# Kernel optimization log

Measured on AMD Instinct MI355X. Metric: run time of the kernel, lower is better.

## Reference

```python
import jax, jax.numpy as jnp
import numpy as np

EPS = 1e-10
B, S, D, K = 8, 2048, 512, 1024
TEMP = 1.0  # quantizer temperature set to 1.0 in SQVAE.__init__


def _ln(x, g, b):
    m = x.mean(-1, keepdims=True)
    v = x.var(-1, keepdims=True)
    return (x - m) / jnp.sqrt(v + 1e-5) * g + b


def _mlp(x, w1, b1, g1, be1, w2, b2, g2, be2):
    # feed_forward: Linear -> ReLU -> LayerNorm, twice (MLPLayers=2)
    h = _ln(jax.nn.relu(x @ w1 + b1), g1, be1)
    return _ln(jax.nn.relu(h @ w2 + b2), g2, be2)


def setup_inputs() -> dict:
    key = jax.random.key(0)
    ks = jax.random.split(key, 20)
    W = 0.04  # small init scale to keep distances / softmax well-conditioned
    p = lambda k, sh, s=1.0: jax.random.normal(k, sh, dtype=jnp.float32) * s
    return {
        'x': p(ks[0], (B, S, D)),
        'gumbel_u': jax.random.uniform(ks[1], (B * S, K), dtype=jnp.float32),
        'enc_w1': p(ks[2], (D, D), W), 'enc_b1': jnp.zeros(D, jnp.float32),
        'enc_g1': jnp.ones(D, jnp.float32), 'enc_be1': jnp.zeros(D, jnp.float32),
        'enc_w2': p(ks[3], (D, D), W), 'enc_b2': jnp.zeros(D, jnp.float32),
        'enc_g2': jnp.ones(D, jnp.float32), 'enc_be2': jnp.zeros(D, jnp.float32),
        'dec_w1': p(ks[4], (D, D), W), 'dec_b1': jnp.zeros(D, jnp.float32),
        'dec_g1': jnp.ones(D, jnp.float32), 'dec_be1': jnp.zeros(D, jnp.float32),
        'dec_w2': p(ks[5], (D, D), W), 'dec_b2': jnp.zeros(D, jnp.float32),
        'dec_g2': jnp.ones(D, jnp.float32), 'dec_be2': jnp.zeros(D, jnp.float32),
        'codebook': p(ks[6], (K, D)),
        'log_param_q': jnp.zeros((), jnp.float32),
    }


def reference(x, gumbel_u, enc_w1, enc_b1, enc_g1, enc_be1, enc_w2, enc_b2, enc_g2, enc_be2,
              dec_w1, dec_b1, dec_g1, dec_be1, dec_w2, dec_b2, dec_g2, dec_be2,
              codebook, log_param_q):
    bs, seq, d = x.shape
    z = _mlp(x, enc_w1, enc_b1, enc_g1, enc_be1, enc_w2, enc_b2, enc_g2, enc_be2)
    # gaussian_1: log_var_q = 0 -> var_q = exp(log_param_q_scalar)
    var_q = jnp.exp(log_param_q)
    w = 0.5 / jnp.clip(var_q, 1e-10)  # 0.5 * precision_q (scalar)
    zf = z.reshape(-1, d)  # [N, D]
    # cdist^2 style distance, scaled by weight -> logits [N, K]
    dist = w * (jnp.sum(zf * zf, axis=1, keepdims=True)
                + jnp.sum(codebook * codebook, axis=1)
                - 2.0 * zf @ codebook.T)
    logit = -dist
    logp = jax.nn.log_softmax(logit, axis=-1)
    probs = jnp.exp(logp)
    # gumbel-softmax sample (train path), noise provided as uniform input
    g = -jnp.log(-jnp.log(gumbel_u + EPS) + EPS)
    encodings = jax.nn.softmax((logit + g) / TEMP, axis=-1)
    z_q = (encodings @ codebook).reshape(bs, seq, d)
    kld_discrete = jnp.sum(probs * logp) / bs
    kld_continuous = jnp.mean(jnp.sum((z - z_q) ** 2 * w, axis=(1, 2)))
    loss = kld_discrete + kld_continuous
    avg_probs = jnp.mean(jax.lax.stop_gradient(probs), axis=0)
    perplexity = jnp.exp(-jnp.sum(avg_probs * jnp.log(avg_probs + 1e-7)))
    x_rec = _mlp(z_q, dec_w1, dec_b1, dec_g1, dec_be1, dec_w2, dec_b2, dec_g2, dec_be2)
    return x_rec, loss, perplexity
```

## Files before the change

### kernel.cpp

```cpp
#include <hip/hip_runtime.h>
#include <math.h>

#define NROWS 16384
#define DIM   512
#define KCODE 1024

typedef __attribute__((ext_vector_type(8))) __bf16 bf16x8;
typedef __attribute__((ext_vector_type(4))) float f32x4;

__device__ __forceinline__ float wave_reduce_sum(float v) {
  #pragma unroll
  for (int m = 1; m < 64; m <<= 1) v += __shfl_xor(v, m, 64);
  return v;
}
__device__ __forceinline__ float wave_reduce_max(float v) {
  #pragma unroll
  for (int m = 1; m < 64; m <<= 1) v = fmaxf(v, __shfl_xor(v, m, 64));
  return v;
}
__device__ __forceinline__ unsigned short f2bf(float f) {
  union { float f; unsigned u; } v; v.f = f;
  unsigned r = v.u + 0x7FFFu + ((v.u >> 16) & 1u);
  return (unsigned short)(r >> 16);
}
__device__ __forceinline__ float bf2f(unsigned short h) {
  union { unsigned u; float f; } v; v.u = ((unsigned)h) << 16;
  return v.f;
}
__device__ __forceinline__ uint4 pack8(const float* x) {
  uint4 r;
  r.x = (unsigned)f2bf(x[0]) | ((unsigned)f2bf(x[1]) << 16);
  r.y = (unsigned)f2bf(x[2]) | ((unsigned)f2bf(x[3]) << 16);
  r.z = (unsigned)f2bf(x[4]) | ((unsigned)f2bf(x[5]) << 16);
  r.w = (unsigned)f2bf(x[6]) | ((unsigned)f2bf(x[7]) << 16);
  return r;
}

__device__ __forceinline__ void glds16(const void* g, void* lds) {
  __builtin_amdgcn_global_load_lds(
      (const __attribute__((address_space(1))) unsigned int*)g,
      (__attribute__((address_space(3))) unsigned int*)lds, 16, 0, 0);
}

__global__ __launch_bounds__(512, 2) void dist_fused(
    const unsigned short* __restrict__ zhp, const unsigned short* __restrict__ zlp,
    const unsigned short* __restrict__ cbh, const unsigned short* __restrict__ cbl,
    const float* __restrict__ znorm, const float* __restrict__ cnorm,
    const float* __restrict__ lpq, float* __restrict__ outf) {
  __shared__ char smem[65536];
  const int t = threadIdx.x;
  const int l = t & 63, w = t >> 6;
  const int wm = w >> 2, wn = w & 3;
  const int b = blockIdx.x;
  const int xcd = b & 7, j = b >> 3;
  const int m0 = (xcd * 8 + j / 4) * 256;
  const int n0 = (j % 4) * 256;

  f32x4 acc[8][4];
  #pragma unroll
  for (int i = 0; i < 8; ++i)
    #pragma unroll
    for (int jj = 0; jj < 4; ++jj) acc[i][jj] = (f32x4){0.f, 0.f, 0.f, 0.f};

  const int row = l & 15;
  const int kcol = (l >> 4) * 8;
  const size_t aLo = (size_t)(m0 + w * 16 + row) * 512 + kcol;
  const size_t aHi = aLo + (size_t)128 * 512;

  const unsigned short* __restrict__ cbhB = cbh + (size_t)(n0 + row) * 512 + kcol;
  const unsigned short* __restrict__ cblB = cbl + (size_t)(n0 + row) * 512 + kcol;

  auto issue = [&](int s) {
    char* hb = smem + (s & 1) * 32768;
    const int kt = s * 32;
    glds16(zhp + aLo + kt, hb + w * 1024);
    glds16(zhp + aHi + kt, hb + (w + 8) * 1024);
    glds16(zlp + aLo + kt, hb + 16384 + w * 1024);
    glds16(zlp + aHi + kt, hb + 16384 + (w + 8) * 1024);
  };

  issue(0);
  #pragma unroll 1
  for (int s = 0; s < 16; ++s) {
    const int kt2 = s * 32;
    bf16x8 bh[4], blf[4];
    #pragma unroll
    for (int i = 0; i < 4; ++i) {
      bh[i]  = *(const bf16x8*)(cbhB + (size_t)(wn * 4 + i) * 8192 + kt2);
      blf[i] = *(const bf16x8*)(cblB + (size_t)(wn * 4 + i) * 8192 + kt2);
    }
    if (s + 1 < 16) {
      issue(s + 1);
      asm volatile("s_waitcnt vmcnt(12)" ::: "memory");
    } else {
      asm volatile("s_waitcnt vmcnt(8)" ::: "memory");
    }
    __builtin_amdgcn_s_barrier();
    const char* hb = smem + (s & 1) * 32768;
    bf16x8 af[8];
    #pragma unroll
    for (int i = 0; i < 8; ++i)
      af[i] = *(const bf16x8*)(hb + (wm * 8 + i) * 1024 + l * 16);
    #pragma unroll
    for (int mi = 0; mi < 8; ++mi)
      #pragma unroll
      for (int ni = 0; ni < 4; ++ni) {
        acc[mi][ni] = __builtin_amdgcn_mfma_f32_16x16x32_bf16(af[mi], bh[ni], acc[mi][ni], 0, 0, 0);
        acc[mi][ni] = __builtin_amdgcn_mfma_f32_16x16x32_bf16(af[mi], blf[ni], acc[mi][ni], 0, 0, 0);
      }
    #pragma unroll
    for (int i = 0; i < 8; ++i)
      af[i] = *(const bf16x8*)(hb + 16384 + (wm * 8 + i) * 1024 + l * 16);
    #pragma unroll
    for (int mi = 0; mi < 8; ++mi)
      #pragma unroll
      for (int ni = 0; ni < 4; ++ni)
        acc[mi][ni] = __builtin_amdgcn_mfma_f32_16x16x32_bf16(af[mi], bh[ni], acc[mi][ni], 0, 0, 0);
    __builtin_amdgcn_s_barrier();
  }

  float* slab = (float*)(smem + w * 4352);
  const int q = l >> 4, c16 = l & 15;
  const int c4 = (l & 15) * 4;
  const float wq = 0.5f / fmaxf(expf(lpq[0]), 1e-10f);

  #pragma unroll
  for (int mi = 0; mi < 8; ++mi) {
    __syncthreads();
    #pragma unroll
    for (int ni = 0; ni < 4; ++ni)
      #pragma unroll
      for (int r = 0; r < 4; ++r)
        slab[(q * 4 + r) * 68 + ni * 16 + c16] = acc[mi][ni][r];
    __syncthreads();
    #pragma unroll
    for (int pp = 0; pp < 4; ++pp) {
      const int rw = pp * 4 + q;
      const float4 v4 = *(const float4*)&slab[rw * 68 + c4];
      const int m = m0 + wm * 128 + mi * 16 + rw;
      const int nc = n0 + wn * 64 + c4;
      const float zn = znorm[m];
      const float4 cn = *(const float4*)&cnorm[nc];
      float4 o;
      o.x = -wq * (zn + cn.x - 2.f * v4.x);
      o.y = -wq * (zn + cn.y - 2.f * v4.y);
      o.z = -wq * (zn + cn.z - 2.f * v4.z);
      o.w = -wq * (zn + cn.w - 2.f * v4.w);
      *(float4*)&outf[(size_t)m * KCODE + nc] = o;
    }
  }
}

template <int EPI, int K, int N, int LDA, int MROWS>
__global__ __launch_bounds__(512, 2) void gemm256(
    const unsigned short* A0, const unsigned short* B0,
    const float* __restrict__ znorm, const float* __restrict__ cnorm,
    const float* __restrict__ lpq,
    const unsigned short* __restrict__ zh, const unsigned short* __restrict__ zl,
    float* __restrict__ kldc,
    unsigned short* __restrict__ outb, float* __restrict__ outf) {
  __shared__ char smem[34816];
  const int t = threadIdx.x;
  const int l = t & 63, w = t >> 6;
  const int wm = w >> 2, wn = w & 3;
  const int NTN = N / 256;
  const int b = blockIdx.x;
  const int xcd = b & 7, j = b >> 3;
  const int MT_PER_XCD = (MROWS / 256) / 8;
  const int m0 = (xcd * MT_PER_XCD + j / NTN) * 256;
  const int n0 = (j % NTN) * 256;

  f32x4 acc[8][4];
  #pragma unroll
  for (int i = 0; i < 8; ++i)
    #pragma unroll
    for (int jj = 0; jj < 4; ++jj) acc[i][jj] = (f32x4){0.f, 0.f, 0.f, 0.f};

  const int row = l & 15;
  const int kcol = (l >> 4) * 8;
  const size_t oA0 = (size_t)(m0 + w * 16 + row) * LDA + kcol;
  const size_t oA1 = oA0 + (size_t)128 * LDA;
  const unsigned short* __restrict__ Bb = B0 + (size_t)(n0 + row) * K + kcol;

  constexpr int NSTEP = K / 32;

  auto issue = [&](int ss) {
    char* hb = smem + (ss & 1) * 16384;
    const int kt = ss * 32;
    glds16(A0 + oA0 + kt, hb + w * 1024);
    glds16(A0 + oA1 + kt, hb + (w + 8) * 1024);
  };

  issue(0);
  #pragma unroll 1
  for (int s = 0; s < NSTEP; ++s) {
    const int kt2 = s * 32;
    bf16x8 bfr[4];
    #pragma unroll
    for (int i = 0; i < 4; ++i)
      bfr[i] = *(const bf16x8*)(Bb + (size_t)(wn * 4 + i) * 16 * K + kt2);
    if (s + 1 < NSTEP) {
      issue(s + 1);
      asm volatile("s_waitcnt vmcnt(6)" ::: "memory");
    } else {
      asm volatile("s_waitcnt vmcnt(4)" ::: "memory");
    }
    __builtin_amdgcn_s_barrier();
    const char* hb = smem + (s & 1) * 16384;
    bf16x8 af[8];
    #pragma unroll
    for (int i = 0; i < 8; ++i)
      af[i] = *(const bf16x8*)(hb + (wm * 8 + i) * 1024 + l * 16);
    #pragma unroll
    for (int mi = 0; mi < 8; ++mi)
      #pragma unroll
      for (int ni = 0; ni < 4; ++ni)
        acc[mi][ni] = __builtin_amdgcn_mfma_f32_16x16x32_bf16(af[mi], bfr[ni], acc[mi][ni], 0, 0, 0);
    __builtin_amdgcn_s_barrier();
  }

  float* slab = (float*)(smem + w * 4352);
  const int q = l >> 4, c16 = l & 15;
  const int c4 = (l & 15) * 4;
  const float wq = 0.5f / fmaxf(expf(lpq[0]), 1e-10f);
  float local = 0.f;

  #pragma unroll
  for (int mi = 0; mi < 8; ++mi) {
    __syncthreads();
    #pragma unroll
    for (int ni = 0; ni < 4; ++ni)
      #pragma unroll
      for (int r = 0; r < 4; ++r)
        slab[(q * 4 + r) * 68 + ni * 16 + c16] = acc[mi][ni][r];
    __syncthreads();
    #pragma unroll
    for (int pp = 0; pp < 4; ++pp) {
      const int rw = pp * 4 + q;
      const float4 v4 = *(const float4*)&slab[rw * 68 + c4];
      float v[4] = {v4.x, v4.y, v4.z, v4.w};
      const int m = m0 + wm * 128 + mi * 16 + rw;
      const int nc = n0 + wn * 64 + c4;
      if (EPI == 1) {
        const float zn = znorm[m];
        const float4 cn = *(const float4*)&cnorm[nc];
        float4 o;
        o.x = -wq * (zn + cn.x - 2.f * v[0]);
        o.y = -wq * (zn + cn.y - 2.f * v[1]);
        o.z = -wq * (zn + cn.z - 2.f * v[2]);
        o.w = -wq * (zn + cn.w - 2.f * v[3]);
        *(float4*)&outf[(size_t)m * N + nc] = o;
      } else {
        const uint2 h2 = *(const uint2*)&zh[(size_t)m * N + nc];
        const uint2 l2 = *(const uint2*)&zl[(size_t)m * N + nc];
        const float z0 = bf2f((unsigned short)(h2.x & 0xFFFF)) + bf2f((unsigned short)(l2.x & 0xFFFF));
        const float z1 = bf2f((unsigned short)(h2.x >> 16))    + bf2f((unsigned short)(l2.x >> 16));
        const float z2 = bf2f((unsigned short)(h2.y & 0xFFFF)) + bf2f((unsigned short)(l2.y & 0xFFFF));
        const float z3 = bf2f((unsigned short)(h2.y >> 16))    + bf2f((unsigned short)(l2.y >> 16));
        const float d0 = z0 - v[0], d1 = z1 - v[1], d2 = z2 - v[2], d3 = z3 - v[3];
        local += d0 * d0 + d1 * d1 + d2 * d2 + d3 * d3;
        uint2 st;
        st.x = (unsigned)f2bf(v[0]) | ((unsigned)f2bf(v[1]) << 16);
        st.y = (unsigned)f2bf(v[2]) | ((unsigned)f2bf(v[3]) << 16);
        *(uint2*)&outb[(size_t)m * N + nc] = st;
      }
    }
  }
  if (EPI == 2) {
    local = wave_reduce_sum(local) * wq;
    if (l == 0) atomicAdd(kldc, local);
  }
}

template <int EPI, int K, int N, int LDA>
__global__ __launch_bounds__(256) void gemm_bt(
    const unsigned short* A0, const unsigned short* B0,
    const float* __restrict__ bias,
    unsigned short* __restrict__ outb) {
  __shared__ char smem[17408];
  const int t = threadIdx.x;
  const int l = t & 63, w = t >> 6;
  const int wm = w >> 1, wn = w & 1;
  const int NTN = N / 128;
  const int b = blockIdx.x;
  const int xcd = b & 7;
  const int j = b >> 3;
  const int m0 = (xcd * 16 + j / NTN) * 128;
  const int n0 = (j % NTN) * 128;

  f32x4 acc[4][4];
  #pragma unroll
  for (int i = 0; i < 4; ++i)
    #pragma unroll
    for (int jj = 0; jj < 4; ++jj) acc[i][jj] = (f32x4){0.f, 0.f, 0.f, 0.f};

  const int row = l & 15;
  const int kcol = (l >> 4) * 8;
  const size_t oA0 = (size_t)(m0 + w * 16 + row) * LDA + kcol;
  const size_t oA1 = oA0 + (size_t)64 * LDA;
  const unsigned short* __restrict__ Bb = B0 + (size_t)(n0 + row) * K + kcol;

  constexpr int NSTEP = K / 32;

  auto issue = [&](int ss) {
    char* hb = smem + (ss & 1) * 8192;
    const int kt = ss * 32;
    glds16(A0 + oA0 + kt, hb + w * 1024);
    glds16(A0 + oA1 + kt, hb + (w + 4) * 1024);
  };

  issue(0);
  #pragma unroll 1
  for (int s = 0; s < NSTEP; ++s) {
    const int kt2 = s * 32;
    bf16x8 bfr[4];
    #pragma unroll
    for (int i = 0; i < 4; ++i)
      bfr[i] = *(const bf16x8*)(Bb + (size_t)(wn * 4 + i) * 16 * K + kt2);
    if (s + 1 < NSTEP) {
      issue(s + 1);
      asm volatile("s_waitcnt vmcnt(6)" ::: "memory");
    } else {
      asm volatile("s_waitcnt vmcnt(4)" ::: "memory");
    }
    __builtin_amdgcn_s_barrier();
    const char* hb = smem + (s & 1) * 8192;
    bf16x8 af[4];
    #pragma unroll
    for (int i = 0; i < 4; ++i)
      af[i] = *(const bf16x8*)(hb + (wm * 4 + i) * 1024 + l * 16);
    #pragma unroll
    for (int mi = 0; mi < 4; ++mi)
      #pragma unroll
      for (int ni = 0; ni < 4; ++ni)
        acc[mi][ni] = __builtin_amdgcn_mfma_f32_16x16x32_bf16(af[mi], bfr[ni], acc[mi][ni], 0, 0, 0);
    __builtin_amdgcn_s_barrier();
  }

  float* slab = (float*)(smem + w * 4352);
  const int q = l >> 4, c16 = l & 15;
  const int c4 = (l & 15) * 4;

  #pragma unroll
  for (int mi = 0; mi < 4; ++mi) {
    __syncthreads();
    #pragma unroll
    for (int ni = 0; ni < 4; ++ni)
      #pragma unroll
      for (int r = 0; r < 4; ++r)
        slab[(q * 4 + r) * 68 + ni * 16 + c16] = acc[mi][ni][r];
    __syncthreads();
    #pragma unroll
    for (int pp = 0; pp < 4; ++pp) {
      const int rw = pp * 4 + q;
      const float4 v4 = *(const float4*)&slab[rw * 68 + c4];
      float v[4] = {v4.x, v4.y, v4.z, v4.w};
      const int m = m0 + wm * 64 + mi * 16 + rw;
      const int nc = n0 + wn * 64 + c4;
      const float4 b4 = *(const float4*)&bias[nc];
      v[0] = fmaxf(v[0] + b4.x, 0.f);
      v[1] = fmaxf(v[1] + b4.y, 0.f);
      v[2] = fmaxf(v[2] + b4.z, 0.f);
      v[3] = fmaxf(v[3] + b4.w, 0.f);
      uint2 st;
      st.x = (unsigned)f2bf(v[0]) | ((unsigned)f2bf(v[1]) << 16);
      st.y = (unsigned)f2bf(v[2]) | ((unsigned)f2bf(v[3]) << 16);
      *(uint2*)&outb[(size_t)m * N + nc] = st;
    }
  }
}

template <int MODE>
__global__ __launch_bounds__(256) void ln_rows(
    const unsigned short* __restrict__ X, const float* __restrict__ g,
    const float* __restrict__ be, unsigned short* __restrict__ Y,
    unsigned short* __restrict__ Yl, float* __restrict__ znorm,
    float* __restrict__ Yf) {
  const int l = threadIdx.x & 63, wv = threadIdx.x >> 6;
  float gv[8], bv[8];
  {
    const float4 a = *(const float4*)&g[l * 8];
    const float4 b = *(const float4*)&g[l * 8 + 4];
    gv[0] = a.x; gv[1] = a.y; gv[2] = a.z; gv[3] = a.w;
    gv[4] = b.x; gv[5] = b.y; gv[6] = b.z; gv[7] = b.w;
    const float4 c = *(const float4*)&be[l * 8];
    const float4 d = *(const float4*)&be[l * 8 + 4];
    bv[0] = c.x; bv[1] = c.y; bv[2] = c.z; bv[3] = c.w;
    bv[4] = d.x; bv[5] = d.y; bv[6] = d.z; bv[7] = d.w;
  }
  const int row0 = blockIdx.x * 32 + wv * 8;
  for (int rr = 0; rr < 8; ++rr) {
    const int row = row0 + rr;
    const uint4 raw = *(const uint4*)&X[(size_t)row * 512 + l * 8];
    float v[8];
    const unsigned rw[4] = {raw.x, raw.y, raw.z, raw.w};
    #pragma unroll
    for (int i = 0; i < 4; ++i) {
      v[2 * i]     = bf2f((unsigned short)(rw[i] & 0xFFFF));
      v[2 * i + 1] = bf2f((unsigned short)(rw[i] >> 16));
    }
    float s = 0.f, ss = 0.f;
    #pragma unroll
    for (int i = 0; i < 8; ++i) { s += v[i]; ss += v[i] * v[i]; }
    #pragma unroll
    for (int m = 1; m < 64; m <<= 1) {
      s += __shfl_xor(s, m, 64);
      ss += __shfl_xor(ss, m, 64);
    }
    const float mean = s * (1.f / 512.f);
    const float var = ss * (1.f / 512.f) - mean * mean;
    const float rstd = rsqrtf(var + 1e-5f);
    float y[8];
    #pragma unroll
    for (int i = 0; i < 8; ++i) y[i] = (v[i] - mean) * rstd * gv[i] + bv[i];
    if (MODE == 0) {
      *(uint4*)&Y[(size_t)row * 512 + l * 8] = pack8(y);
    } else if (MODE == 1) {
      float lo[8], ns = 0.f;
      unsigned short hx[8];
      #pragma unroll
      for (int i = 0; i < 8; ++i) {
        hx[i] = f2bf(y[i]);
        lo[i] = y[i] - bf2f(hx[i]);
        ns += y[i] * y[i];
      }
      uint4 hv;
      hv.x = (unsigned)hx[0] | ((unsigned)hx[1] << 16);
      hv.y = (unsigned)hx[2] | ((unsigned)hx[3] << 16);
      hv.z = (unsigned)hx[4] | ((unsigned)hx[5] << 16);
      hv.w = (unsigned)hx[6] | ((unsigned)hx[7] << 16);
      *(uint4*)&Y[(size_t)row * 512 + l * 8] = hv;
      *(uint4*)&Yl[(size_t)row * 512 + l * 8] = pack8(lo);
      ns = wave_reduce_sum(ns);
      if (l == 0) znorm[row] = ns;
    } else {
      float4 o0, o1;
      o0.x = y[0]; o0.y = y[1]; o0.z = y[2]; o0.w = y[3];
      o1.x = y[4]; o1.y = y[5]; o1.z = y[6]; o1.w = y[7];
      *(float4*)&Yf[(size_t)row * 512 + l * 8] = o0;
      *(float4*)&Yf[(size_t)row * 512 + l * 8 + 4] = o1;
    }
  }
}

__global__ __launch_bounds__(256) void convert_f32_bf16(
    const float* __restrict__ X, unsigned short* __restrict__ Y) {
  const size_t i = ((size_t)blockIdx.x * 256 + threadIdx.x) * 8;
  const float4 a = *(const float4*)&X[i];
  const float4 b = *(const float4*)&X[i + 4];
  float v[8] = {a.x, a.y, a.z, a.w, b.x, b.y, b.z, b.w};
  *(uint4*)&Y[i] = pack8(v);
}

__global__ __launch_bounds__(256) void prep_cb(
    const float* __restrict__ CB, unsigned short* __restrict__ H,
    unsigned short* __restrict__ L, float* __restrict__ cnorm) {
  const int wv = threadIdx.x >> 6, l = threadIdx.x & 63;
  const int r = blockIdx.x * 4 + wv;
  const float* row = &CB[(size_t)r * 512 + l * 8];
  const float4 a = *(const float4*)row;
  const float4 b = *(const float4*)(row + 4);
  float x[8] = {a.x, a.y, a.z, a.w, b.x, b.y, b.z, b.w};
  float s = 0.f, lo[8];
  unsigned short hi[8];
  #pragma unroll
  for (int i = 0; i < 8; ++i) {
    s += x[i] * x[i];
    hi[i] = f2bf(x[i]);
    lo[i] = x[i] - bf2f(hi[i]);
  }
  uint4 hv;
  hv.x = (unsigned)hi[0] | ((unsigned)hi[1] << 16);
  hv.y = (unsigned)hi[2] | ((unsigned)hi[3] << 16);
  hv.z = (unsigned)hi[4] | ((unsigned)hi[5] << 16);
  hv.w = (unsigned)hi[6] | ((unsigned)hi[7] << 16);
  *(uint4*)&H[(size_t)r * 512 + l * 8] = hv;
  *(uint4*)&L[(size_t)r * 512 + l * 8] = pack8(lo);
  s = wave_reduce_sum(s);
  if (l == 0) cnorm[r] = s;
}

__global__ __launch_bounds__(256) void transpose_f32_bf16(
    const float* __restrict__ in, unsigned short* __restrict__ out, int R, int C) {
  __shared__ float tile[32][33];
  const int ntc = C >> 5;
  const int c0 = (blockIdx.x % ntc) * 32, r0 = (blockIdx.x / ntc) * 32;
  const int tx = threadIdx.x & 31, ty = threadIdx.x >> 5;
  #pragma unroll
  for (int i = 0; i < 4; ++i)
    tile[ty + 8 * i][tx] = in[(size_t)(r0 + ty + 8 * i) * C + c0 + tx];
  __syncthreads();
  #pragma unroll
  for (int i = 0; i < 4; ++i)
    out[(size_t)(c0 + ty + 8 * i) * R + r0 + tx] = f2bf(tile[tx][ty + 8 * i]);
}

__global__ __launch_bounds__(256) void softmax_gumbel(
    const float* logits, const float* __restrict__ U, unsigned short* E,
    float* __restrict__ colsum, float* __restrict__ kldd_acc) {
  __shared__ float cs[1024];
  __shared__ float kd[4];
  const int t = threadIdx.x;
  const int wv = t >> 6, l = t & 63;
  #pragma unroll
  for (int i = 0; i < 4; ++i) cs[t + 256 * i] = 0.f;
  __syncthreads();
  float psum[16];
  #pragma unroll
  for (int i = 0; i < 16; ++i) psum[i] = 0.f;
  float kldd = 0.f;
  const int nbase = blockIdx.x * 16 + wv * 4;

  for (int it = 0; it < 4; ++it) {
    const int row = nbase + it;
    const size_t off = (size_t)row * KCODE + 4 * l;
    float v[16];
    #pragma unroll
    for (int jj = 0; jj < 4; ++jj) {
      const float4 t4 = *(const float4*)&logits[off + 256 * jj];
      v[4 * jj + 0] = t4.x; v[4 * jj + 1] = t4.y; v[4 * jj + 2] = t4.z; v[4 * jj + 3] = t4.w;
    }
    float m = v[0];
    #pragma unroll
    for (int i = 1; i < 16; ++i) m = fmaxf(m, v[i]);
    m = wave_reduce_max(m);
    float e[16], se = 0.f;
    #pragma unroll
    for (int i = 0; i < 16; ++i) { e[i] = __expf(v[i] - m); se += e[i]; }
    se = wave_reduce_sum(se);
    const float lz = __logf(se);
    const float inv_se = 1.f / se;
    float pl = 0.f;
    #pragma unroll
    for (int i = 0; i < 16; ++i) {
      const float p = e[i] * inv_se;
      psum[i] += p;
      pl += p * (v[i] - m - lz);
    }
    kldd += pl;
    float y[16];
    #pragma unroll
    for (int jj = 0; jj < 4; ++jj) {
      const float4 t4 = *(const float4*)&U[off + 256 * jj];
      y[4 * jj + 0] = v[4 * jj + 0] - __logf(-__logf(t4.x + 1e-10f) + 1e-10f);
      y[4 * jj + 1] = v[4 * jj + 1] - __logf(-__logf(t4.y + 1e-10f) + 1e-10f);
      y[4 * jj + 2] = v[4 * jj + 2] - __logf(-__logf(t4.z + 1e-10f) + 1e-10f);
      y[4 * jj + 3] = v[4 * jj + 3] - __logf(-__logf(t4.w + 1e-10f) + 1e-10f);
    }
    float m2 = y[0];
    #pragma unroll
    for (int i = 1; i < 16; ++i) m2 = fmaxf(m2, y[i]);
    m2 = wave_reduce_max(m2);
    float ey[16], s2 = 0.f;
    #pragma unroll
    for (int i = 0; i < 16; ++i) { ey[i] = __expf(y[i] - m2); s2 += ey[i]; }
    s2 = wave_reduce_sum(s2);
    const float inv = 1.f / s2;
    #pragma unroll
    for (int jj = 0; jj < 4; ++jj) {
      ushort4 e4;
      e4.x = f2bf(ey[4 * jj + 0] * inv);
      e4.y = f2bf(ey[4 * jj + 1] * inv);
      e4.z = f2bf(ey[4 * jj + 2] * inv);
      e4.w = f2bf(ey[4 * jj + 3] * inv);
      *(ushort4*)&E[(size_t)row * 2048 + 4 * l + 256 * jj] = e4;
    }
  }
  #pragma unroll
  for (int jj = 0; jj < 4; ++jj)
    #pragma unroll
    for (int c = 0; c < 4; ++c)
      atomicAdd(&cs[256 * jj + 4 * l + c], psum[4 * jj + c]);
  kldd = wave_reduce_sum(kldd);
  if (l == 0) kd[wv] = kldd;
  __syncthreads();
  #pragma unroll
  for (int i = 0; i < 4; ++i) {
    const float vv = cs[t + 256 * i];
    if (vv != 0.f) atomicAdd(&colsum[t + 256 * i], vv);
  }
  if (t == 0) atomicAdd(kldd_acc, kd[0] + kd[1] + kd[2] + kd[3]);
}

__global__ __launch_bounds__(256) void finalize(
    const float* __restrict__ colsum, const float* __restrict__ scal,
    float* __restrict__ out) {
  const int t = threadIdx.x;
  float ent = 0.f;
  #pragma unroll
  for (int jj = 0; jj < 4; ++jj) {
    const float a = colsum[t + 256 * jj] * (1.f / 16384.f);
    ent += a * logf(a + 1e-7f);
  }
  ent = wave_reduce_sum(ent);
  __shared__ float red[4];
  if ((t & 63) == 0) red[t >> 6] = ent;
  __syncthreads();
  if (t == 0) {
    const float tot = red[0] + red[1] + red[2] + red[3];
    out[0] = (scal[0] + scal[1]) * (1.f / 8.f);
    out[1] = expf(-tot);
  }
}

extern "C" void kernel_launch(void* const* d_in, const int* in_sizes, int n_in,
                              void* d_out, int out_size, void* d_ws, size_t ws_size,
                              hipStream_t stream) {
  const float* x      = (const float*)d_in[0];
  const float* gu     = (const float*)d_in[1];
  const float* enc_w1 = (const float*)d_in[2];
  const float* enc_b1 = (const float*)d_in[3];
  const float* enc_g1 = (const float*)d_in[4];
  const float* enc_e1 = (const float*)d_in[5];
  const float* enc_w2 = (const float*)d_in[6];
  const float* enc_b2 = (const float*)d_in[7];
  const float* enc_g2 = (const float*)d_in[8];
  const float* enc_e2 = (const float*)d_in[9];
  const float* dec_w1 = (const float*)d_in[10];
  const float* dec_b1 = (const float*)d_in[11];
  const float* dec_g1 = (const float*)d_in[12];
  const float* dec_e1 = (const float*)d_in[13];
  const float* dec_w2 = (const float*)d_in[14];
  const float* dec_b2 = (const float*)d_in[15];
  const float* dec_g2 = (const float*)d_in[16];
  const float* dec_e2 = (const float*)d_in[17];
  const float* cb     = (const float*)d_in[18];
  const float* lpq    = (const float*)d_in[19];
  float* out = (float*)d_out;
  char* wsb = (char*)d_ws;

  float*          logits = (float*)(wsb + 0);
  unsigned short* Eb     = (unsigned short*)(wsb + 0);
  unsigned short* t1     = (unsigned short*)(wsb + 67108864);
  unsigned short* xb     = (unsigned short*)(wsb + 83886080);
  unsigned short* zh     = xb;
  unsigned short* hq     = (unsigned short*)(wsb + 100663296);
  unsigned short* zl     = (unsigned short*)(wsb + 117440512);
  unsigned short* wt0    = (unsigned short*)(wsb + 134217728);
  unsigned short* wt1    = wt0 + 262144;
  unsigned short* wt2    = wt1 + 262144;
  unsigned short* wt3    = wt2 + 262144;
  unsigned short* cbh    = (unsigned short*)(wsb + 136314880);
  unsigned short* cbl    = (unsigned short*)(wsb + 137363456);
  unsigned short* cbT    = (unsigned short*)(wsb + 138412032);
  float*          znorm  = (float*)(wsb + 139460608);
  float*          cnorm  = (float*)(wsb + 139526144);
  float*          colsum = (float*)(wsb + 139530240);
  float*          scal   = (float*)(wsb + 139534336);

  hipMemsetAsync(colsum, 0, 4096 + 16, stream);

  convert_f32_bf16<<<4096, 256, 0, stream>>>(x, xb);
  prep_cb<<<256, 256, 0, stream>>>(cb, cbh, cbl, cnorm);
  transpose_f32_bf16<<<256, 256, 0, stream>>>(enc_w1, wt0, 512, 512);
  transpose_f32_bf16<<<256, 256, 0, stream>>>(enc_w2, wt1, 512, 512);
  transpose_f32_bf16<<<256, 256, 0, stream>>>(dec_w1, wt2, 512, 512);
  transpose_f32_bf16<<<256, 256, 0, stream>>>(dec_w2, wt3, 512, 512);
  transpose_f32_bf16<<<512, 256, 0, stream>>>(cb, cbT, 1024, 512);

  gemm_bt<0, 512, 512, 512><<<512, 256, 0, stream>>>(xb, wt0, enc_b1, t1);
  ln_rows<0><<<512, 256, 0, stream>>>(t1, enc_g1, enc_e1, hq, nullptr, nullptr, nullptr);
  gemm_bt<0, 512, 512, 512><<<512, 256, 0, stream>>>(hq, wt1, enc_b2, t1);
  ln_rows<1><<<512, 256, 0, stream>>>(t1, enc_g2, enc_e2, zh, zl, znorm, nullptr);
  dist_fused<<<256, 512, 0, stream>>>(
      zh, zl, cbh, cbl, znorm, cnorm, lpq, logits);
  softmax_gumbel<<<1024, 256, 0, stream>>>(logits, gu, Eb, colsum, &scal[0]);
  gemm256<2, 1024, 512, 2048, 16384><<<128, 512, 0, stream>>>(
      Eb, cbT, nullptr, nullptr, lpq, zh, zl, &scal[1], hq, nullptr);
  gemm_bt<0, 512, 512, 512><<<512, 256, 0, stream>>>(hq, wt2, dec_b1, t1);
  ln_rows<0><<<512, 256, 0, stream>>>(t1, dec_g1, dec_e1, zl, nullptr, nullptr, nullptr);
  gemm_bt<0, 512, 512, 512><<<512, 256, 0, stream>>>(zl, wt3, dec_b2, t1);
  ln_rows<2><<<512, 256, 0, stream>>>(t1, dec_g2, dec_e2, nullptr, nullptr, nullptr, out);
  finalize<<<1, 256, 0, stream>>>(colsum, scal, out + 8388608);
}
```

Before: 524.1 us.

## Stage codebook/weight operands through LDS and merge GEMM kernels into one template

The distance kernel now loads both z and codebook hi/lo tiles into LDS with 64-wide K steps (128KB smem, single-buffered with a full vmcnt(0) wait) instead of reading B fragments directly from global memory. The 128x128 gemm_bt kernel is rewritten to stage B through LDS as well, with 64-wide K steps and double buffering, and it absorbs the encodings@codebook GEMM epilogue, replacing the 256x256 gemm256 kernel with 512 smaller blocks. This aims to cut redundant global loads and improve occupancy for the z_q GEMM. The trade-off is that the distance kernel loses load/compute overlap and its larger LDS footprint may limit occupancy.

New measurement: 469.9 us. 1.12x faster.

```diff
diff --git a/kernel.cpp b/kernel.cpp
--- a/kernel.cpp
+++ b/kernel.cpp
@@ -47,7 +47,7 @@
     const unsigned short* __restrict__ cbh, const unsigned short* __restrict__ cbl,
     const float* __restrict__ znorm, const float* __restrict__ cnorm,
     const float* __restrict__ lpq, float* __restrict__ outf) {
-  __shared__ char smem[65536];
+  __shared__ char smem[131072];
   const int t = threadIdx.x;
   const int l = t & 63, w = t >> 6;
   const int wm = w >> 2, wn = w & 3;
@@ -66,56 +66,56 @@
   const int kcol = (l >> 4) * 8;
   const size_t aLo = (size_t)(m0 + w * 16 + row) * 512 + kcol;
   const size_t aHi = aLo + (size_t)128 * 512;
-
-  const unsigned short* __restrict__ cbhB = cbh + (size_t)(n0 + row) * 512 + kcol;
-  const unsigned short* __restrict__ cblB = cbl + (size_t)(n0 + row) * 512 + kcol;
-
-  auto issue = [&](int s) {
-    char* hb = smem + (s & 1) * 32768;
-    const int kt = s * 32;
-    glds16(zhp + aLo + kt, hb + w * 1024);
-    glds16(zhp + aHi + kt, hb + (w + 8) * 1024);
-    glds16(zlp + aLo + kt, hb + 16384 + w * 1024);
-    glds16(zlp + aHi + kt, hb + 16384 + (w + 8) * 1024);
-  };
-
-  issue(0);
+  const size_t bLo = (size_t)(n0 + w * 16 + row) * 512 + kcol;
+  const size_t bHi = bLo + (size_t)128 * 512;
+  const int dLo = w * 2048, dHi = (w + 8) * 2048;
+
   #pragma unroll 1
-  for (int s = 0; s < 16; ++s) {
-    const int kt2 = s * 32;
-    bf16x8 bh[4], blf[4];
-    #pragma unroll
-    for (int i = 0; i < 4; ++i) {
-      bh[i]  = *(const bf16x8*)(cbhB + (size_t)(wn * 4 + i) * 8192 + kt2);
-      blf[i] = *(const bf16x8*)(cblB + (size_t)(wn * 4 + i) * 8192 + kt2);
-    }
-    if (s + 1 < 16) {
-      issue(s + 1);
-      asm volatile("s_waitcnt vmcnt(12)" ::: "memory");
-    } else {
-      asm volatile("s_waitcnt vmcnt(8)" ::: "memory");
-    }
+  for (int s = 0; s < 8; ++s) {
+    const int kt = s * 64;
+    #pragma unroll
+    for (int js = 0; js < 2; ++js) {
+      const int ko = kt + js * 32;
+      const int dj = js * 1024;
+      glds16(zhp + aLo + ko, smem + dLo + dj);
+      glds16(zhp + aHi + ko, smem + dHi + dj);
+      glds16(zlp + aLo + ko, smem + 32768 + dLo + dj);
+      glds16(zlp + aHi + ko, smem + 32768 + dHi + dj);
+      glds16(cbh + bLo + ko, smem + 65536 + dLo + dj);
+      glds16(cbh + bHi + ko, smem + 65536 + dHi + dj);
+      glds16(cbl + bLo + ko, smem + 98304 + dLo + dj);
+      glds16(cbl + bHi + ko, smem + 98304 + dHi + dj);
+    }
+    asm volatile("s_waitcnt vmcnt(0)" ::: "memory");
     __builtin_amdgcn_s_barrier();
-    const char* hb = smem + (s & 1) * 32768;
-    bf16x8 af[8];
-    #pragma unroll
-    for (int i = 0; i < 8; ++i)
-      af[i] = *(const bf16x8*)(hb + (wm * 8 + i) * 1024 + l * 16);
-    #pragma unroll
-    for (int mi = 0; mi < 8; ++mi)
-      #pragma unroll
-      for (int ni = 0; ni < 4; ++ni) {
-        acc[mi][ni] = __builtin_amdgcn_mfma_f32_16x16x32_bf16(af[mi], bh[ni], acc[mi][ni], 0, 0, 0);
-        acc[mi][ni] = __builtin_amdgcn_mfma_f32_16x16x32_bf16(af[mi], blf[ni], acc[mi][ni], 0, 0, 0);
+    #pragma unroll
+    for (int js = 0; js < 2; ++js) {
+      const int dj = js * 1024;
+      bf16x8 af[8], bh_[4], bl_[4];
+      #pragma unroll
+      for (int i = 0; i < 4; ++i) {
+        bh_[i] = *(const bf16x8*)(smem + 65536 + (wn * 4 + i) * 2048 + dj + l * 16);
+        bl_[i] = *(const bf16x8*)(smem + 98304 + (wn * 4 + i) * 2048 + dj + l * 16);
       }
-    #pragma unroll
-    for (int i = 0; i < 8; ++i)
-      af[i] = *(const bf16x8*)(hb + 16384 + (wm * 8 + i) * 1024 + l * 16);
-    #pragma unroll
-    for (int mi = 0; mi < 8; ++mi)
-      #pragma unroll
-      for (int ni = 0; ni < 4; ++ni)
-        acc[mi][ni] = __builtin_amdgcn_mfma_f32_16x16x32_bf16(af[mi], bh[ni], acc[mi][ni], 0, 0, 0);
+      #pragma unroll
+      for (int i = 0; i < 8; ++i)
+        af[i] = *(const bf16x8*)(smem + (wm * 8 + i) * 2048 + dj + l * 16);
+      #pragma unroll
+      for (int mi = 0; mi < 8; ++mi)
+        #pragma unroll
+        for (int ni = 0; ni < 4; ++ni) {
+          acc[mi][ni] = __builtin_amdgcn_mfma_f32_16x16x32_bf16(af[mi], bh_[ni], acc[mi][ni], 0, 0, 0);
+          acc[mi][ni] = __builtin_amdgcn_mfma_f32_16x16x32_bf16(af[mi], bl_[ni], acc[mi][ni], 0, 0, 0);
+        }
+      #pragma unroll
+      for (int i = 0; i < 8; ++i)
+        af[i] = *(const bf16x8*)(smem + 32768 + (wm * 8 + i) * 2048 + dj + l * 16);
+      #pragma unroll
+      for (int mi = 0; mi < 8; ++mi)
+        #pragma unroll
+        for (int ni = 0; ni < 4; ++ni)
+          acc[mi][ni] = __builtin_amdgcn_mfma_f32_16x16x32_bf16(af[mi], bh_[ni], acc[mi][ni], 0, 0, 0);
+    }
     __builtin_amdgcn_s_barrier();
   }
 
@@ -151,82 +151,90 @@
   }
 }
 
-template <int EPI, int K, int N, int LDA, int MROWS>
-__global__ __launch_bounds__(512, 2) void gemm256(
+template <int EPI, int K, int N, int LDA>
+__global__ __launch_bounds__(256) void gemm_bt(
     const unsigned short* A0, const unsigned short* B0,
-    const float* __restrict__ znorm, const float* __restrict__ cnorm,
-    const float* __restrict__ lpq,
+    const float* __restrict__ bias, const float* __restrict__ lpq,
     const unsigned short* __restrict__ zh, const unsigned short* __restrict__ zl,
-    float* __restrict__ kldc,
-    unsigned short* __restrict__ outb, float* __restrict__ outf) {
-  __shared__ char smem[34816];
+    float* __restrict__ kldc, unsigned short* __restrict__ outb) {
+  __shared__ char smem[65536];
   const int t = threadIdx.x;
   const int l = t & 63, w = t >> 6;
-  const int wm = w >> 2, wn = w & 3;
-  const int NTN = N / 256;
+  const int wm = w >> 1, wn = w & 1;
+  const int NTN = N / 128;
   const int b = blockIdx.x;
-  const int xcd = b & 7, j = b >> 3;
-  const int MT_PER_XCD = (MROWS / 256) / 8;
-  const int m0 = (xcd * MT_PER_XCD + j / NTN) * 256;
-  const int n0 = (j % NTN) * 256;
-
-  f32x4 acc[8][4];
-  #pragma unroll
-  for (int i = 0; i < 8; ++i)
+  const int xcd = b & 7;
+  const int j = b >> 3;
+  const int m0 = (xcd * 16 + j / NTN) * 128;
+  const int n0 = (j % NTN) * 128;
+
+  f32x4 acc[4][4];
+  #pragma unroll
+  for (int i = 0; i < 4; ++i)
     #pragma unroll
     for (int jj = 0; jj < 4; ++jj) acc[i][jj] = (f32x4){0.f, 0.f, 0.f, 0.f};
 
   const int row = l & 15;
   const int kcol = (l >> 4) * 8;
   const size_t oA0 = (size_t)(m0 + w * 16 + row) * LDA + kcol;
-  const size_t oA1 = oA0 + (size_t)128 * LDA;
-  const unsigned short* __restrict__ Bb = B0 + (size_t)(n0 + row) * K + kcol;
-
-  constexpr int NSTEP = K / 32;
+  const size_t oA1 = oA0 + (size_t)64 * LDA;
+  const size_t oB0 = (size_t)(n0 + w * 16 + row) * K + kcol;
+  const size_t oB1 = oB0 + (size_t)64 * K;
+  const int dLo = w * 2048, dHi = (w + 4) * 2048;
+
+  constexpr int NSTEP = K / 64;
 
   auto issue = [&](int ss) {
-    char* hb = smem + (ss & 1) * 16384;
-    const int kt = ss * 32;
-    glds16(A0 + oA0 + kt, hb + w * 1024);
-    glds16(A0 + oA1 + kt, hb + (w + 8) * 1024);
+    char* hb = smem + (ss & 1) * 32768;
+    const int kt = ss * 64;
+    #pragma unroll
+    for (int js = 0; js < 2; ++js) {
+      const int ko = kt + js * 32;
+      const int dj = js * 1024;
+      glds16(A0 + oA0 + ko, hb + dLo + dj);
+      glds16(A0 + oA1 + ko, hb + dHi + dj);
+      glds16(B0 + oB0 + ko, hb + 16384 + dLo + dj);
+      glds16(B0 + oB1 + ko, hb + 16384 + dHi + dj);
+    }
   };
 
   issue(0);
   #pragma unroll 1
   for (int s = 0; s < NSTEP; ++s) {
-    const int kt2 = s * 32;
-    bf16x8 bfr[4];
-    #pragma unroll
-    for (int i = 0; i < 4; ++i)
-      bfr[i] = *(const bf16x8*)(Bb + (size_t)(wn * 4 + i) * 16 * K + kt2);
     if (s + 1 < NSTEP) {
       issue(s + 1);
-      asm volatile("s_waitcnt vmcnt(6)" ::: "memory");
+      asm volatile("s_waitcnt vmcnt(8)" ::: "memory");
     } else {
-      asm volatile("s_waitcnt vmcnt(4)" ::: "memory");
+      asm volatile("s_waitcnt vmcnt(0)" ::: "memory");
     }
     __builtin_amdgcn_s_barrier();
-    const char* hb = smem + (s & 1) * 16384;
-    bf16x8 af[8];
-    #pragma unroll
-    for (int i = 0; i < 8; ++i)
-      af[i] = *(const bf16x8*)(hb + (wm * 8 + i) * 1024 + l * 16);
-    #pragma unroll
-    for (int mi = 0; mi < 8; ++mi)
-      #pragma unroll
-      for (int ni = 0; ni < 4; ++ni)
-        acc[mi][ni] = __builtin_amdgcn_mfma_f32_16x16x32_bf16(af[mi], bfr[ni], acc[mi][ni], 0, 0, 0);
+    const char* hb = smem + (s & 1) * 32768;
+    #pragma unroll
+    for (int js = 0; js < 2; ++js) {
+      const int dj = js * 1024;
+      bf16x8 af[4], bfr[4];
+      #pragma unroll
+      for (int i = 0; i < 4; ++i) {
+        af[i]  = *(const bf16x8*)(hb + (wm * 4 + i) * 2048 + dj + l * 16);
+        bfr[i] = *(const bf16x8*)(hb + 16384 + (wn * 4 + i) * 2048 + dj + l * 16);
+      }
+      #pragma unroll
+      for (int mi = 0; mi < 4; ++mi)
+        #pragma unroll
+        for (int ni = 0; ni < 4; ++ni)
+          acc[mi][ni] = __builtin_amdgcn_mfma_f32_16x16x32_bf16(af[mi], bfr[ni], acc[mi][ni], 0, 0, 0);
+    }
     __builtin_amdgcn_s_barrier();
   }
 
   float* slab = (float*)(smem + w * 4352);
   const int q = l >> 4, c16 = l & 15;
   const int c4 = (l & 15) * 4;
-  const float wq = 0.5f / fmaxf(expf(lpq[0]), 1e-10f);
+  const float wq = (EPI == 2) ? 0.5f / fmaxf(expf(lpq[0]), 1e-10f) : 0.f;
   float local = 0.f;
 
   #pragma unroll
-  for (int mi = 0; mi < 8; ++mi) {
+  for (int mi = 0; mi < 4; ++mi) {
     __syncthreads();
     #pragma unroll
     for (int ni = 0; ni < 4; ++ni)
@@ -239,17 +247,18 @@
       const int rw = pp * 4 + q;
       const float4 v4 = *(const float4*)&slab[rw * 68 + c4];
       float v[4] = {v4.x, v4.y, v4.z, v4.w};
-      const int m = m0 + wm * 128 + mi * 16 + rw;
+      const int m = m0 + wm * 64 + mi * 16 + rw;
       const int nc = n0 + wn * 64 + c4;
-      if (EPI == 1) {
-        const float zn = znorm[m];
-        const float4 cn = *(const float4*)&cnorm[nc];
-        float4 o;
-        o.x = -wq * (zn + cn.x - 2.f * v[0]);
-        o.y = -wq * (zn + cn.y - 2.f * v[1]);
-        o.z = -wq * (zn + cn.z - 2.f * v[2]);
-        o.w = -wq * (zn + cn.w - 2.f * v[3]);
-        *(float4*)&outf[(size_t)m * N + nc] = o;
+      if (EPI == 0) {
+        const float4 b4 = *(const float4*)&bias[nc];
+        v[0] = fmaxf(v[0] + b4.x, 0.f);
+        v[1] = fmaxf(v[1] + b4.y, 0.f);
+        v[2] = fmaxf(v[2] + b4.z, 0.f);
+        v[3] = fmaxf(v[3] + b4.w, 0.f);
+        uint2 st;
+        st.x = (unsigned)f2bf(v[0]) | ((unsigned)f2bf(v[1]) << 16);
+        st.y = (unsigned)f2bf(v[2]) | ((unsigned)f2bf(v[3]) << 16);
+        *(uint2*)&outb[(size_t)m * N + nc] = st;
       } else {
         const uint2 h2 = *(const uint2*)&zh[(size_t)m * N + nc];
         const uint2 l2 = *(const uint2*)&zl[(size_t)m * N + nc];
@@ -269,104 +278,6 @@
   if (EPI == 2) {
     local = wave_reduce_sum(local) * wq;
     if (l == 0) atomicAdd(kldc, local);
-  }
-}
-
-template <int EPI, int K, int N, int LDA>
-__global__ __launch_bounds__(256) void gemm_bt(
-    const unsigned short* A0, const unsigned short* B0,
-    const float* __restrict__ bias,
-    unsigned short* __restrict__ outb) {
-  __shared__ char smem[17408];
-  const int t = threadIdx.x;
-  const int l = t & 63, w = t >> 6;
-  const int wm = w >> 1, wn = w & 1;
-  const int NTN = N / 128;
-  const int b = blockIdx.x;
-  const int xcd = b & 7;
-  const int j = b >> 3;
-  const int m0 = (xcd * 16 + j / NTN) * 128;
-  const int n0 = (j % NTN) * 128;
-
-  f32x4 acc[4][4];
-  #pragma unroll
-  for (int i = 0; i < 4; ++i)
-    #pragma unroll
-    for (int jj = 0; jj < 4; ++jj) acc[i][jj] = (f32x4){0.f, 0.f, 0.f, 0.f};
-
-  const int row = l & 15;
-  const int kcol = (l >> 4) * 8;
-  const size_t oA0 = (size_t)(m0 + w * 16 + row) * LDA + kcol;
-  const size_t oA1 = oA0 + (size_t)64 * LDA;
-  const unsigned short* __restrict__ Bb = B0 + (size_t)(n0 + row) * K + kcol;
-
-  constexpr int NSTEP = K / 32;
-
-  auto issue = [&](int ss) {
-    char* hb = smem + (ss & 1) * 8192;
-    const int kt = ss * 32;
-    glds16(A0 + oA0 + kt, hb + w * 1024);
-    glds16(A0 + oA1 + kt, hb + (w + 4) * 1024);
-  };
-
-  issue(0);
-  #pragma unroll 1
-  for (int s = 0; s < NSTEP; ++s) {
-    const int kt2 = s * 32;
-    bf16x8 bfr[4];
-    #pragma unroll
-    for (int i = 0; i < 4; ++i)
-      bfr[i] = *(const bf16x8*)(Bb + (size_t)(wn * 4 + i) * 16 * K + kt2);
-    if (s + 1 < NSTEP) {
-      issue(s + 1);
-      asm volatile("s_waitcnt vmcnt(6)" ::: "memory");
-    } else {
-      asm volatile("s_waitcnt vmcnt(4)" ::: "memory");
-    }
-    __builtin_amdgcn_s_barrier();
-    const char* hb = smem + (s & 1) * 8192;
-    bf16x8 af[4];
-    #pragma unroll
-    for (int i = 0; i < 4; ++i)
-      af[i] = *(const bf16x8*)(hb + (wm * 4 + i) * 1024 + l * 16);
-    #pragma unroll
-    for (int mi = 0; mi < 4; ++mi)
-      #pragma unroll
-      for (int ni = 0; ni < 4; ++ni)
-        acc[mi][ni] = __builtin_amdgcn_mfma_f32_16x16x32_bf16(af[mi], bfr[ni], acc[mi][ni], 0, 0, 0);
-    __builtin_amdgcn_s_barrier();
-  }
-
-  float* slab = (float*)(smem + w * 4352);
-  const int q = l >> 4, c16 = l & 15;
-  const int c4 = (l & 15) * 4;
-
-  #pragma unroll
-  for (int mi = 0; mi < 4; ++mi) {
-    __syncthreads();
-    #pragma unroll
-    for (int ni = 0; ni < 4; ++ni)
-      #pragma unroll
-      for (int r = 0; r < 4; ++r)
-        slab[(q * 4 + r) * 68 + ni * 16 + c16] = acc[mi][ni][r];
-    __syncthreads();
-    #pragma unroll
-    for (int pp = 0; pp < 4; ++pp) {
-      const int rw = pp * 4 + q;
-      const float4 v4 = *(const float4*)&slab[rw * 68 + c4];
-      float v[4] = {v4.x, v4.y, v4.z, v4.w};
-      const int m = m0 + wm * 64 + mi * 16 + rw;
-      const int nc = n0 + wn * 64 + c4;
-      const float4 b4 = *(const float4*)&bias[nc];
-      v[0] = fmaxf(v[0] + b4.x, 0.f);
-      v[1] = fmaxf(v[1] + b4.y, 0.f);
-      v[2] = fmaxf(v[2] + b4.z, 0.f);
-      v[3] = fmaxf(v[3] + b4.w, 0.f);
-      uint2 st;
-      st.x = (unsigned)f2bf(v[0]) | ((unsigned)f2bf(v[1]) << 16);
-      st.y = (unsigned)f2bf(v[2]) | ((unsigned)f2bf(v[3]) << 16);
-      *(uint2*)&outb[(size_t)m * N + nc] = st;
-    }
   }
 }
 
@@ -658,18 +569,22 @@
   transpose_f32_bf16<<<256, 256, 0, stream>>>(dec_w2, wt3, 512, 512);
   transpose_f32_bf16<<<512, 256, 0, stream>>>(cb, cbT, 1024, 512);
 
-  gemm_bt<0, 512, 512, 512><<<512, 256, 0, stream>>>(xb, wt0, enc_b1, t1);
+  gemm_bt<0, 512, 512, 512><<<512, 256, 0, stream>>>(
+      xb, wt0, enc_b1, nullptr, nullptr, nullptr, nullptr, t1);
   ln_rows<0><<<512, 256, 0, stream>>>(t1, enc_g1, enc_e1, hq, nullptr, nullptr, nullptr);
-  gemm_bt<0, 512, 512, 512><<<512, 256, 0, stream>>>(hq, wt1, enc_b2, t1);
+  gemm_bt<0, 512, 512, 512><<<512, 256, 0, stream>>>(
+      hq, wt1, enc_b2, nullptr, nullptr, nullptr, nullptr, t1);
   ln_rows<1><<<512, 256, 0, stream>>>(t1, enc_g2, enc_e2, zh, zl, znorm, nullptr);
   dist_fused<<<256, 512, 0, stream>>>(
       zh, zl, cbh, cbl, znorm, cnorm, lpq, logits);
   softmax_gumbel<<<1024, 256, 0, stream>>>(logits, gu, Eb, colsum, &scal[0]);
-  gemm256<2, 1024, 512, 2048, 16384><<<128, 512, 0, stream>>>(
-      Eb, cbT, nullptr, nullptr, lpq, zh, zl, &scal[1], hq, nullptr);
-  gemm_bt<0, 512, 512, 512><<<512, 256, 0, stream>>>(hq, wt2, dec_b1, t1);
+  gemm_bt<2, 1024, 512, 2048><<<512, 256, 0, stream>>>(
+      Eb, cbT, nullptr, lpq, zh, zl, &scal[1], hq);
+  gemm_bt<0, 512, 512, 512><<<512, 256, 0, stream>>>(
+      hq, wt2, dec_b1, nullptr, nullptr, nullptr, nullptr, t1);
   ln_rows<0><<<512, 256, 0, stream>>>(t1, dec_g1, dec_e1, zl, nullptr, nullptr, nullptr);
-  gemm_bt<0, 512, 512, 512><<<512, 256, 0, stream>>>(zl, wt3, dec_b2, t1);
+  gemm_bt<0, 512, 512, 512><<<512, 256, 0, stream>>>(
+      zl, wt3, dec_b2, nullptr, nullptr, nullptr, nullptr, t1);
   ln_rows<2><<<512, 256, 0, stream>>>(t1, dec_g2, dec_e2, nullptr, nullptr, nullptr, out);
   finalize<<<1, 256, 0, stream>>>(colsum, scal, out + 8388608);
 }
```
